# Kernel tuning notes

Hardware: AMD Instinct MI355X
Metric: run time of the kernel (lower is better)

The kernel has to match this reference:

```python
import jax, jax.numpy as jnp
import numpy as np

B, N, D, H = 4, 2048, 1024, 16
HD = D // H
SCALE = D ** -0.5  # NOTE: original scales by dimension**-0.5 (not head_dim**-0.5)


def setup_inputs() -> dict:
    key = jax.random.key(0)
    k1, k2, k3 = jax.random.split(key, 3)
    x = jax.random.normal(k1, (B, N, D), dtype=jnp.float32)
    w_qkv = jax.random.normal(k2, (D, 3 * D), dtype=jnp.float32) * (D ** -0.5)
    w_proj = jax.random.normal(k3, (D, D), dtype=jnp.float32) * (D ** -0.5)
    b_proj = jnp.zeros((D,), dtype=jnp.float32)
    return {"x": x, "w_qkv": w_qkv, "w_proj": w_proj, "b_proj": b_proj}


def reference(x, w_qkv, w_proj, b_proj):
    # qkv projection: [B,N,3D] -> split into q,k,v each [B,H,N,HD]
    qkv = x @ w_qkv
    qkv = qkv.reshape(B, N, 3, H, HD).transpose(2, 0, 3, 1, 4)  # [3,B,H,N,HD]
    q, k, v = qkv[0], qkv[1], qkv[2]
    scores = jnp.einsum('bhid,bhjd->bhij', q, k) * SCALE
    attn = jax.nn.softmax(scores, axis=-1)
    out = jnp.einsum('bhij,bhjd->bhid', attn, v)  # [B,H,N,HD]
    out = out.transpose(0, 2, 1, 3).reshape(B, N, D)
    return out @ w_proj + b_proj
```

## Files before the change

kernel.cpp:

```cpp
#include <hip/hip_runtime.h>
#include <stdint.h>

#define Bdim 4
#define Nseq 2048
#define Dmod 1024
#define Hn   16
#define HD   64
#define SCALE 0.03125f
#define L2E   1.44269504089f

typedef __attribute__((ext_vector_type(8))) short short8;
typedef __attribute__((ext_vector_type(8))) unsigned short ushort8;
typedef __attribute__((ext_vector_type(4))) float f32x4;
typedef __attribute__((ext_vector_type(16))) float f32x16;

typedef __attribute__((address_space(3))) uint32_t lds_u32;
typedef __attribute__((address_space(1))) const uint32_t glob_u32;

static __device__ __forceinline__ void gload_lds16(const unsigned short* g, unsigned short* l) {
    __builtin_amdgcn_global_load_lds((glob_u32*)(const void*)g, (lds_u32*)(void*)l, 16, 0, 0);
}

static __device__ __forceinline__ unsigned short f2bf(float f) {
    union { float f; uint32_t u; } v; v.f = f;
    uint32_t r = (v.u + 0x7FFFu + ((v.u >> 16) & 1u)) >> 16;
    return (unsigned short)r;
}

__global__ __launch_bounds__(256) void cast_x_kernel(const float* __restrict__ in,
                                                     unsigned short* __restrict__ out, int n4) {
    int i = blockIdx.x * blockDim.x + threadIdx.x;
    int stride = gridDim.x * blockDim.x;
    for (; i < n4; i += stride) {
        float4 v = reinterpret_cast<const float4*>(in)[i];
        ushort4 o;
        o.x = f2bf(v.x); o.y = f2bf(v.y); o.z = f2bf(v.z); o.w = f2bf(v.w);
        reinterpret_cast<ushort4*>(out)[i] = o;
    }
}

__global__ void transpose_cast_kernel(const float* __restrict__ in,
                                      unsigned short* __restrict__ out, int R, int C) {
    __shared__ unsigned short t[32][33];
    int c0 = blockIdx.x * 32, r0 = blockIdx.y * 32;
    int tx = threadIdx.x, ty = threadIdx.y;
#pragma unroll
    for (int i = 0; i < 4; ++i)
        t[ty + i*8][tx] = f2bf(in[(size_t)(r0 + ty + i*8) * C + c0 + tx]);
    __syncthreads();
#pragma unroll
    for (int i = 0; i < 4; ++i)
        out[(size_t)(c0 + ty + i*8) * R + r0 + tx] = t[tx][ty + i*8];
}

template<bool OUT_BF16, bool BIAS>
__global__ __launch_bounds__(256) void gemm_bt_kernel(const unsigned short* __restrict__ A,
                                                      const unsigned short* __restrict__ Bt,
                                                      void* __restrict__ Cv,
                                                      const float* __restrict__ bias,
                                                      int M, int N, int K) {
    __shared__ unsigned short Al[128 * 64];
    __shared__ unsigned short Bl[128 * 64];
    int tid = threadIdx.x;
    int lane = tid & 63, wv = tid >> 6;
    int wr = (wv >> 1) * 64, wc = (wv & 1) * 64;
    int lr = lane & 15, lg = lane >> 4, lk = lg * 8;

    int gx = gridDim.x;
    int lin = blockIdx.y * gx + blockIdx.x;
    int cpx = (gx * gridDim.y) >> 3;
    int nl = (lin & 7) * cpx + (lin >> 3);
    int m0 = (nl / gx) * 128, n0 = (nl % gx) * 128;

    int srow = wv * 8 + (lane >> 3);
    int scol = (lane & 7) * 8;
    const unsigned short* ag = A  + (size_t)(m0 + srow) * K + scol;
    const unsigned short* bg = Bt + (size_t)(n0 + srow) * K + scol;
    unsigned short* la = Al + wv * 512;
    unsigned short* lb = Bl + wv * 512;

    f32x4 acc[4][4];
#pragma unroll
    for (int i = 0; i < 4; ++i)
#pragma unroll
        for (int j = 0; j < 4; ++j) acc[i][j] = (f32x4)0.f;

    for (int k0 = 0; k0 < K; k0 += 64) {
        __syncthreads();
#pragma unroll
        for (int i = 0; i < 4; ++i) {
            gload_lds16(ag + (size_t)i * 32 * K + k0, la + i * 2048);
            gload_lds16(bg + (size_t)i * 32 * K + k0, lb + i * 2048);
        }
        __syncthreads();
#pragma unroll
        for (int ks = 0; ks < 2; ++ks) {
            short8 a[4], b[4];
#pragma unroll
            for (int mi = 0; mi < 4; ++mi)
                a[mi] = *reinterpret_cast<const short8*>(Al + (wr + mi*16 + lr) * 64 + ks*32 + lk);
#pragma unroll
            for (int nj = 0; nj < 4; ++nj)
                b[nj] = *reinterpret_cast<const short8*>(Bl + (wc + nj*16 + lr) * 64 + ks*32 + lk);
#pragma unroll
            for (int mi = 0; mi < 4; ++mi)
#pragma unroll
                for (int nj = 0; nj < 4; ++nj)
                    acc[mi][nj] = __builtin_amdgcn_mfma_f32_16x16x32_bf16(a[mi], b[nj], acc[mi][nj], 0, 0, 0);
        }
    }
#pragma unroll
    for (int mi = 0; mi < 4; ++mi) {
#pragma unroll
        for (int nj = 0; nj < 4; ++nj) {
            int r = m0 + wr + mi*16 + lg*4;
            int c = n0 + wc + nj*16 + lr;
            float bv = BIAS ? bias[c] : 0.f;
#pragma unroll
            for (int i = 0; i < 4; ++i) {
                float v = acc[mi][nj][i] + bv;
                if (OUT_BF16)
                    reinterpret_cast<unsigned short*>(Cv)[(size_t)(r + i) * N + c] = f2bf(v);
                else
                    reinterpret_cast<float*>(Cv)[(size_t)(r + i) * N + c] = v;
            }
        }
    }
}

__global__ __launch_bounds__(256) void transpose_v_kernel(const unsigned short* __restrict__ qkv,
                                                          unsigned short* __restrict__ vT) {
    __shared__ unsigned short t[64][68];
    int bh = blockIdx.y, b = bh >> 4, h = bh & 15;
    int j0 = blockIdx.x * 64;
    int tid = threadIdx.x;
#pragma unroll
    for (int p = 0; p < 4; ++p) {
        int e = p * 256 + tid;
        int jj = e >> 4;
        int d4 = (e & 15) * 4;
        const unsigned short* src = qkv + (size_t)(b*Nseq + j0 + jj) * 3072 + 2048 + h*64 + d4;
        ushort4 v = *reinterpret_cast<const ushort4*>(src);
        *reinterpret_cast<ushort4*>(&t[jj][d4]) = v;
    }
    __syncthreads();
#pragma unroll
    for (int p = 0; p < 4; ++p) {
        int e = p * 256 + tid;
        int d = e >> 4;
        int j4 = (e & 15) * 4;
        ushort4 v;
        v.x = t[j4 + 0][d]; v.y = t[j4 + 1][d]; v.z = t[j4 + 2][d]; v.w = t[j4 + 3][d];
        *reinterpret_cast<ushort4*>(vT + ((size_t)bh * 64 + d) * Nseq + j0 + j4) = v;
    }
}

__global__ __launch_bounds__(256, 2) void attn_kernel(const unsigned short* __restrict__ qkv,
                                                      const unsigned short* __restrict__ vT,
                                                      unsigned short* __restrict__ attn_o) {
    __shared__ unsigned short Kl[2 * 64 * 64];
    __shared__ unsigned short Vl[2 * 64 * 64];
    __shared__ unsigned short Pl[4 * 64 * 64];

    int w = blockIdx.x;
    int lid = (w & 7) * 64 + (w >> 3);
    int bh = lid >> 3, qb = lid & 7;
    int b = bh >> 4, h = bh & 15;

    int tid = threadIdx.x, lane = tid & 63, wv = tid >> 6;
    int lr = lane & 31, hi = lane >> 5;
    int q0 = qb * 256 + wv * 64;

    short8 qfA[4], qfB[4];
    {
        const unsigned short* qrowA = qkv + (size_t)(b * Nseq + q0 + lr) * 3072 + h * 64 + hi * 8;
        const unsigned short* qrowB = qrowA + (size_t)32 * 3072;
#pragma unroll
        for (int ks = 0; ks < 4; ++ks) {
            qfA[ks] = *reinterpret_cast<const short8*>(qrowA + ks * 16);
            qfB[ks] = *reinterpret_cast<const short8*>(qrowB + ks * 16);
        }
    }

    float mrunA = -1e30f, lrunA = 0.f, mrunB = -1e30f, lrunB = 0.f;
    f32x16 oA0 = (f32x16)0.f, oA1 = (f32x16)0.f, oB0 = (f32x16)0.f, oB1 = (f32x16)0.f;

    int sr = tid >> 2;
    int sc = (tid & 3) * 32;
    const unsigned short* kg = qkv + (size_t)(b * Nseq + sr) * 3072 + 1024 + h * 64 + sc / 2;
    const unsigned short* vg = vT + ((size_t)(bh * 64 + sr)) * Nseq + sc / 2;
    int swz0 = sr * 128 + ((sc) ^ ((sr & 7) << 4));
    int swz1 = sr * 128 + ((sc + 16) ^ ((sr & 7) << 4));
    int rswz = (lr & 7) << 4;
    char* PlW = (char*)Pl + wv * 8192 + lr * 128;

    {
        ushort8 a0 = *reinterpret_cast<const ushort8*>(kg);
        ushort8 a1 = *reinterpret_cast<const ushort8*>(kg + 8);
        ushort8 a2 = *reinterpret_cast<const ushort8*>(vg);
        ushort8 a3 = *reinterpret_cast<const ushort8*>(vg + 8);
        *reinterpret_cast<ushort8*>((char*)Kl + swz0) = a0;
        *reinterpret_cast<ushort8*>((char*)Kl + swz1) = a1;
        *reinterpret_cast<ushort8*>((char*)Vl + swz0) = a2;
        *reinterpret_cast<ushort8*>((char*)Vl + swz1) = a3;
    }
    ushort8 k0r = *reinterpret_cast<const ushort8*>(kg + (size_t)64 * 3072);
    ushort8 k1r = *reinterpret_cast<const ushort8*>(kg + (size_t)64 * 3072 + 8);
    ushort8 v0r = *reinterpret_cast<const ushort8*>(vg + 64);
    ushort8 v1r = *reinterpret_cast<const ushort8*>(vg + 72);

    int cur = 0;
    for (int jt = 0; jt < Nseq; jt += 64, cur ^= 1) {
        __syncthreads();
        int rb = cur * 8192, wb = rb ^ 8192;

        f32x16 sA0 = (f32x16)0.f, sA1 = (f32x16)0.f, sB0 = (f32x16)0.f, sB1 = (f32x16)0.f;
        __builtin_amdgcn_s_setprio(1);
#pragma unroll
        for (int ks = 0; ks < 4; ++ks) {
            int cb = ks * 32 + hi * 16;
            short8 kf0 = *reinterpret_cast<const short8*>((char*)Kl + rb + lr * 128 + (cb ^ rswz));
            short8 kf1 = *reinterpret_cast<const short8*>((char*)Kl + rb + (lr + 32) * 128 + (cb ^ rswz));
            sA0 = __builtin_amdgcn_mfma_f32_32x32x16_bf16(kf0, qfA[ks], sA0, 0, 0, 0);
            sA1 = __builtin_amdgcn_mfma_f32_32x32x16_bf16(kf1, qfA[ks], sA1, 0, 0, 0);
            sB0 = __builtin_amdgcn_mfma_f32_32x32x16_bf16(kf0, qfB[ks], sB0, 0, 0, 0);
            sB1 = __builtin_amdgcn_mfma_f32_32x32x16_bf16(kf1, qfB[ks], sB1, 0, 0, 0);
        }
        __builtin_amdgcn_s_setprio(0);

        if (jt + 64 < Nseq) {
            *reinterpret_cast<ushort8*>((char*)Kl + wb + swz0) = k0r;
            *reinterpret_cast<ushort8*>((char*)Kl + wb + swz1) = k1r;
            *reinterpret_cast<ushort8*>((char*)Vl + wb + swz0) = v0r;
            *reinterpret_cast<ushort8*>((char*)Vl + wb + swz1) = v1r;
            int jn = jt + 128;
            if (jn < Nseq) {
                k0r = *reinterpret_cast<const ushort8*>(kg + (size_t)jn * 3072);
                k1r = *reinterpret_cast<const ushort8*>(kg + (size_t)jn * 3072 + 8);
                v0r = *reinterpret_cast<const ushort8*>(vg + jn);
                v1r = *reinterpret_cast<const ushort8*>(vg + jn + 8);
            }
        }

        float tA[16], tB[16];
#pragma unroll
        for (int i = 0; i < 16; ++i) { tA[i] = fmaxf(sA0[i], sA1[i]); tB[i] = fmaxf(sB0[i], sB1[i]); }
#pragma unroll
        for (int st = 8; st > 0; st >>= 1)
#pragma unroll
            for (int i = 0; i < st; ++i) { tA[i] = fmaxf(tA[i], tA[i + st]); tB[i] = fmaxf(tB[i], tB[i + st]); }
        float mlocA = fmaxf(tA[0], __shfl_xor(tA[0], 32)) * SCALE;
        float mlocB = fmaxf(tB[0], __shfl_xor(tB[0], 32)) * SCALE;

        if (!__all((mlocA <= mrunA + 8.f) && (mlocB <= mrunB + 8.f))) {
            float mnA = fmaxf(mrunA, mlocA);
            float fA = __builtin_amdgcn_exp2f((mrunA - mnA) * L2E);
            float mnB = fmaxf(mrunB, mlocB);
            float fB = __builtin_amdgcn_exp2f((mrunB - mnB) * L2E);
            lrunA *= fA; lrunB *= fB; mrunA = mnA; mrunB = mnB;
#pragma unroll
            for (int i = 0; i < 16; ++i) {
                oA0[i] *= fA; oA1[i] *= fA; oB0[i] *= fB; oB1[i] *= fB;
            }
        }

        const float c1 = SCALE * L2E;
        float c0A = -mrunA * L2E, c0B = -mrunB * L2E;
        float pA0[16], pA1[16], pB0[16], pB1[16];
#pragma unroll
        for (int i = 0; i < 16; ++i) {
            pA0[i] = __builtin_amdgcn_exp2f(fmaf(sA0[i], c1, c0A));
            pA1[i] = __builtin_amdgcn_exp2f(fmaf(sA1[i], c1, c0A));
            pB0[i] = __builtin_amdgcn_exp2f(fmaf(sB0[i], c1, c0B));
            pB1[i] = __builtin_amdgcn_exp2f(fmaf(sB1[i], c1, c0B));
        }

        uint32_t WA[16], WB[16];
#pragma unroll
        for (int m = 0; m < 8; ++m) {
            asm("v_cvt_pk_bf16_f32 %0, %1, %2" : "=v"(WA[m])   : "v"(pA0[2*m]), "v"(pA0[2*m+1]));
            asm("v_cvt_pk_bf16_f32 %0, %1, %2" : "=v"(WA[8+m]) : "v"(pA1[2*m]), "v"(pA1[2*m+1]));
            asm("v_cvt_pk_bf16_f32 %0, %1, %2" : "=v"(WB[m])   : "v"(pB0[2*m]), "v"(pB0[2*m+1]));
            asm("v_cvt_pk_bf16_f32 %0, %1, %2" : "=v"(WB[8+m]) : "v"(pB1[2*m]), "v"(pB1[2*m+1]));
        }
#pragma unroll
        for (int tt = 0; tt < 8; ++tt) {
            uint64_t valA = (uint64_t)WA[2*tt] | ((uint64_t)WA[2*tt+1] << 32);
            uint64_t valB = (uint64_t)WB[2*tt] | ((uint64_t)WB[2*tt+1] << 32);
            int off = (16*tt + 8*hi) ^ rswz;
            *reinterpret_cast<uint64_t*>(PlW + off) = valA;
            *reinterpret_cast<uint64_t*>(PlW + 4096 + off) = valB;
        }

        float aA[16], aB[16];
#pragma unroll
        for (int i = 0; i < 16; ++i) { aA[i] = pA0[i] + pA1[i]; aB[i] = pB0[i] + pB1[i]; }
#pragma unroll
        for (int st = 8; st > 0; st >>= 1)
#pragma unroll
            for (int i = 0; i < st; ++i) { aA[i] += aA[i + st]; aB[i] += aB[i + st]; }
        lrunA += aA[0] + __shfl_xor(aA[0], 32);
        lrunB += aB[0] + __shfl_xor(aB[0], 32);

        __builtin_amdgcn_s_setprio(1);
#pragma unroll
        for (int ks4 = 0; ks4 < 4; ++ks4) {
            int cb = ks4 * 32 + hi * 16;
            short8 vf0 = *reinterpret_cast<const short8*>((char*)Vl + rb + lr * 128 + (cb ^ rswz));
            short8 vf1 = *reinterpret_cast<const short8*>((char*)Vl + rb + (lr + 32) * 128 + (cb ^ rswz));
            short8 pfA = *reinterpret_cast<const short8*>(PlW + (cb ^ rswz));
            short8 pfB = *reinterpret_cast<const short8*>(PlW + 4096 + (cb ^ rswz));
            oA0 = __builtin_amdgcn_mfma_f32_32x32x16_bf16(vf0, pfA, oA0, 0, 0, 0);
            oA1 = __builtin_amdgcn_mfma_f32_32x32x16_bf16(vf1, pfA, oA1, 0, 0, 0);
            oB0 = __builtin_amdgcn_mfma_f32_32x32x16_bf16(vf0, pfB, oB0, 0, 0, 0);
            oB1 = __builtin_amdgcn_mfma_f32_32x32x16_bf16(vf1, pfB, oB1, 0, 0, 0);
        }
        __builtin_amdgcn_s_setprio(0);
    }

    float invA = 1.f / lrunA, invB = 1.f / lrunB;
    unsigned short* orowA = attn_o + (size_t)(b * Nseq + q0 + lr) * Dmod + h * 64;
    unsigned short* orowB = attn_o + (size_t)(b * Nseq + q0 + 32 + lr) * Dmod + h * 64;
#pragma unroll
    for (int db = 0; db < 2; ++db)
#pragma unroll
        for (int g = 0; g < 4; ++g) {
            int d = db * 32 + 8 * g + 4 * hi;
            ushort4 o4;
            o4.x = f2bf((db ? oA1[4*g+0] : oA0[4*g+0]) * invA);
            o4.y = f2bf((db ? oA1[4*g+1] : oA0[4*g+1]) * invA);
            o4.z = f2bf((db ? oA1[4*g+2] : oA0[4*g+2]) * invA);
            o4.w = f2bf((db ? oA1[4*g+3] : oA0[4*g+3]) * invA);
            *reinterpret_cast<ushort4*>(orowA + d) = o4;
            o4.x = f2bf((db ? oB1[4*g+0] : oB0[4*g+0]) * invB);
            o4.y = f2bf((db ? oB1[4*g+1] : oB0[4*g+1]) * invB);
            o4.z = f2bf((db ? oB1[4*g+2] : oB0[4*g+2]) * invB);
            o4.w = f2bf((db ? oB1[4*g+3] : oB0[4*g+3]) * invB);
            *reinterpret_cast<ushort4*>(orowB + d) = o4;
        }
}

extern "C" void kernel_launch(void* const* d_in, const int* in_sizes, int n_in,
                              void* d_out, int out_size, void* d_ws, size_t ws_size,
                              hipStream_t stream) {
    const float* x      = (const float*)d_in[0];
    const float* w_qkv  = (const float*)d_in[1];
    const float* w_proj = (const float*)d_in[2];
    const float* b_proj = (const float*)d_in[3];
    float* out = (float*)d_out;
    char* ws = (char*)d_ws;

    unsigned short* qkv    = (unsigned short*)(ws);
    unsigned short* vT     = (unsigned short*)(ws + 50331648);
    unsigned short* xb     = (unsigned short*)(ws + 67108864);
    unsigned short* attn_o = xb;
    unsigned short* wqkvT  = (unsigned short*)(ws + 83886080);
    unsigned short* wprojT = (unsigned short*)(ws + 90177536);

    cast_x_kernel<<<2048, 256, 0, stream>>>(x, xb, (Bdim*Nseq*Dmod)/4);
    transpose_cast_kernel<<<dim3(3072/32, 1024/32), dim3(32, 8), 0, stream>>>(w_qkv, wqkvT, 1024, 3072);
    transpose_cast_kernel<<<dim3(1024/32, 1024/32), dim3(32, 8), 0, stream>>>(w_proj, wprojT, 1024, 1024);
    gemm_bt_kernel<true, false><<<dim3(3072/128, 8192/128), 256, 0, stream>>>(
        xb, wqkvT, qkv, nullptr, Bdim*Nseq, 3*Dmod, Dmod);
    transpose_v_kernel<<<dim3(Nseq/64, Bdim*Hn), 256, 0, stream>>>(qkv, vT);
    attn_kernel<<<512, 256, 0, stream>>>(qkv, vT, attn_o);
    gemm_bt_kernel<false, true><<<dim3(1024/128, 8192/128), 256, 0, stream>>>(
        attn_o, wprojT, out, b_proj, Bdim*Nseq, Dmod, Dmod);
}
```

Measured before the change: 226.2 us.

## Fuse V transpose into QKV GEMM epilogue and remap attention LDS layout

The QKV GEMM epilogue now writes the V columns straight into the transposed vT buffer, so the separate transpose_v kernel launch and its extra read/write of V are gone. The attention kernel's K, V and P shared-memory tiles change from an XOR-swizzled row layout to a fragment-major layout where each lane reads a contiguous 16 bytes. This is meant to simplify address math and avoid bank conflicts. The vT stores from the GEMM are 8-byte scattered writes with a large stride, which may cost some write efficiency.

```diff
diff --git a/kernel.cpp b/kernel.cpp
--- a/kernel.cpp
+++ b/kernel.cpp
@@ -53,11 +53,12 @@
         out[(size_t)(c0 + ty + i*8) * R + r0 + tx] = t[tx][ty + i*8];
 }
 
-template<bool OUT_BF16, bool BIAS>
+template<bool OUT_BF16, bool BIAS, bool VSPLIT>
 __global__ __launch_bounds__(256) void gemm_bt_kernel(const unsigned short* __restrict__ A,
                                                       const unsigned short* __restrict__ Bt,
                                                       void* __restrict__ Cv,
                                                       const float* __restrict__ bias,
+                                                      unsigned short* __restrict__ vTp,
                                                       int M, int N, int K) {
     __shared__ unsigned short Al[128 * 64];
     __shared__ unsigned short Bl[128 * 64];
@@ -115,43 +116,28 @@
         for (int nj = 0; nj < 4; ++nj) {
             int r = m0 + wr + mi*16 + lg*4;
             int c = n0 + wc + nj*16 + lr;
-            float bv = BIAS ? bias[c] : 0.f;
-#pragma unroll
-            for (int i = 0; i < 4; ++i) {
-                float v = acc[mi][nj][i] + bv;
-                if (OUT_BF16)
-                    reinterpret_cast<unsigned short*>(Cv)[(size_t)(r + i) * N + c] = f2bf(v);
-                else
-                    reinterpret_cast<float*>(Cv)[(size_t)(r + i) * N + c] = v;
+            if (VSPLIT && c >= 2048) {
+                int cc = c - 2048;
+                int bh = ((r >> 11) << 4) + (cc >> 6);
+                int d = cc & 63;
+                ushort4 o4;
+                o4.x = f2bf(acc[mi][nj][0]);
+                o4.y = f2bf(acc[mi][nj][1]);
+                o4.z = f2bf(acc[mi][nj][2]);
+                o4.w = f2bf(acc[mi][nj][3]);
+                *reinterpret_cast<ushort4*>(vTp + ((size_t)(bh * 64 + d) * 2048) + (r & 2047)) = o4;
+            } else {
+                float bv = BIAS ? bias[c] : 0.f;
+#pragma unroll
+                for (int i = 0; i < 4; ++i) {
+                    float v = acc[mi][nj][i] + bv;
+                    if (OUT_BF16)
+                        reinterpret_cast<unsigned short*>(Cv)[(size_t)(r + i) * N + c] = f2bf(v);
+                    else
+                        reinterpret_cast<float*>(Cv)[(size_t)(r + i) * N + c] = v;
+                }
             }
         }
-    }
-}
-
-__global__ __launch_bounds__(256) void transpose_v_kernel(const unsigned short* __restrict__ qkv,
-                                                          unsigned short* __restrict__ vT) {
-    __shared__ unsigned short t[64][68];
-    int bh = blockIdx.y, b = bh >> 4, h = bh & 15;
-    int j0 = blockIdx.x * 64;
-    int tid = threadIdx.x;
-#pragma unroll
-    for (int p = 0; p < 4; ++p) {
-        int e = p * 256 + tid;
-        int jj = e >> 4;
-        int d4 = (e & 15) * 4;
-        const unsigned short* src = qkv + (size_t)(b*Nseq + j0 + jj) * 3072 + 2048 + h*64 + d4;
-        ushort4 v = *reinterpret_cast<const ushort4*>(src);
-        *reinterpret_cast<ushort4*>(&t[jj][d4]) = v;
-    }
-    __syncthreads();
-#pragma unroll
-    for (int p = 0; p < 4; ++p) {
-        int e = p * 256 + tid;
-        int d = e >> 4;
-        int j4 = (e & 15) * 4;
-        ushort4 v;
-        v.x = t[j4 + 0][d]; v.y = t[j4 + 1][d]; v.z = t[j4 + 2][d]; v.w = t[j4 + 3][d];
-        *reinterpret_cast<ushort4*>(vT + ((size_t)bh * 64 + d) * Nseq + j0 + j4) = v;
     }
 }
 
@@ -186,23 +172,21 @@
     f32x16 oA0 = (f32x16)0.f, oA1 = (f32x16)0.f, oB0 = (f32x16)0.f, oB1 = (f32x16)0.f;
 
     int sr = tid >> 2;
-    int sc = (tid & 3) * 32;
-    const unsigned short* kg = qkv + (size_t)(b * Nseq + sr) * 3072 + 1024 + h * 64 + sc / 2;
-    const unsigned short* vg = vT + ((size_t)(bh * 64 + sr)) * Nseq + sc / 2;
-    int swz0 = sr * 128 + ((sc) ^ ((sr & 7) << 4));
-    int swz1 = sr * 128 + ((sc + 16) ^ ((sr & 7) << 4));
-    int rswz = (lr & 7) << 4;
-    char* PlW = (char*)Pl + wv * 8192 + lr * 128;
+    const unsigned short* kg = qkv + (size_t)(b * Nseq + sr) * 3072 + 1024 + h * 64 + (tid & 3) * 16;
+    const unsigned short* vg = vT + ((size_t)(bh * 64 + sr)) * Nseq + (tid & 3) * 16;
+    int sb = (sr >> 5) * 4096 + (tid & 3) * 1024 + (sr & 31) * 16;
+    char* Pw = (char*)Pl + wv * 8192 + lr * 16 + 8 * hi;
+    char* Pr = (char*)Pl + wv * 8192 + lane * 16;
 
     {
         ushort8 a0 = *reinterpret_cast<const ushort8*>(kg);
         ushort8 a1 = *reinterpret_cast<const ushort8*>(kg + 8);
         ushort8 a2 = *reinterpret_cast<const ushort8*>(vg);
         ushort8 a3 = *reinterpret_cast<const ushort8*>(vg + 8);
-        *reinterpret_cast<ushort8*>((char*)Kl + swz0) = a0;
-        *reinterpret_cast<ushort8*>((char*)Kl + swz1) = a1;
-        *reinterpret_cast<ushort8*>((char*)Vl + swz0) = a2;
-        *reinterpret_cast<ushort8*>((char*)Vl + swz1) = a3;
+        *reinterpret_cast<ushort8*>((char*)Kl + sb) = a0;
+        *reinterpret_cast<ushort8*>((char*)Kl + sb + 512) = a1;
+        *reinterpret_cast<ushort8*>((char*)Vl + sb) = a2;
+        *reinterpret_cast<ushort8*>((char*)Vl + sb + 512) = a3;
     }
     ushort8 k0r = *reinterpret_cast<const ushort8*>(kg + (size_t)64 * 3072);
     ushort8 k1r = *reinterpret_cast<const ushort8*>(kg + (size_t)64 * 3072 + 8);
@@ -218,9 +202,8 @@
         __builtin_amdgcn_s_setprio(1);
 #pragma unroll
         for (int ks = 0; ks < 4; ++ks) {
-            int cb = ks * 32 + hi * 16;
-            short8 kf0 = *reinterpret_cast<const short8*>((char*)Kl + rb + lr * 128 + (cb ^ rswz));
-            short8 kf1 = *reinterpret_cast<const short8*>((char*)Kl + rb + (lr + 32) * 128 + (cb ^ rswz));
+            short8 kf0 = *reinterpret_cast<const short8*>((char*)Kl + rb + ks*1024 + lane*16);
+            short8 kf1 = *reinterpret_cast<const short8*>((char*)Kl + rb + 4096 + ks*1024 + lane*16);
             sA0 = __builtin_amdgcn_mfma_f32_32x32x16_bf16(kf0, qfA[ks], sA0, 0, 0, 0);
             sA1 = __builtin_amdgcn_mfma_f32_32x32x16_bf16(kf1, qfA[ks], sA1, 0, 0, 0);
             sB0 = __builtin_amdgcn_mfma_f32_32x32x16_bf16(kf0, qfB[ks], sB0, 0, 0, 0);
@@ -229,10 +212,10 @@
         __builtin_amdgcn_s_setprio(0);
 
         if (jt + 64 < Nseq) {
-            *reinterpret_cast<ushort8*>((char*)Kl + wb + swz0) = k0r;
-            *reinterpret_cast<ushort8*>((char*)Kl + wb + swz1) = k1r;
-            *reinterpret_cast<ushort8*>((char*)Vl + wb + swz0) = v0r;
-            *reinterpret_cast<ushort8*>((char*)Vl + wb + swz1) = v1r;
+            *reinterpret_cast<ushort8*>((char*)Kl + wb + sb) = k0r;
+            *reinterpret_cast<ushort8*>((char*)Kl + wb + sb + 512) = k1r;
+            *reinterpret_cast<ushort8*>((char*)Vl + wb + sb) = v0r;
+            *reinterpret_cast<ushort8*>((char*)Vl + wb + sb + 512) = v1r;
             int jn = jt + 128;
             if (jn < Nseq) {
                 k0r = *reinterpret_cast<const ushort8*>(kg + (size_t)jn * 3072);
@@ -287,9 +270,9 @@
         for (int tt = 0; tt < 8; ++tt) {
             uint64_t valA = (uint64_t)WA[2*tt] | ((uint64_t)WA[2*tt+1] << 32);
             uint64_t valB = (uint64_t)WB[2*tt] | ((uint64_t)WB[2*tt+1] << 32);
-            int off = (16*tt + 8*hi) ^ rswz;
-            *reinterpret_cast<uint64_t*>(PlW + off) = valA;
-            *reinterpret_cast<uint64_t*>(PlW + 4096 + off) = valB;
+            char* pa = Pw + (tt >> 1) * 1024 + (tt & 1) * 512;
+            *reinterpret_cast<uint64_t*>(pa) = valA;
+            *reinterpret_cast<uint64_t*>(pa + 4096) = valB;
         }
 
         float aA[16], aB[16];
@@ -305,11 +288,10 @@
         __builtin_amdgcn_s_setprio(1);
 #pragma unroll
         for (int ks4 = 0; ks4 < 4; ++ks4) {
-            int cb = ks4 * 32 + hi * 16;
-            short8 vf0 = *reinterpret_cast<const short8*>((char*)Vl + rb + lr * 128 + (cb ^ rswz));
-            short8 vf1 = *reinterpret_cast<const short8*>((char*)Vl + rb + (lr + 32) * 128 + (cb ^ rswz));
-            short8 pfA = *reinterpret_cast<const short8*>(PlW + (cb ^ rswz));
-            short8 pfB = *reinterpret_cast<const short8*>(PlW + 4096 + (cb ^ rswz));
+            short8 vf0 = *reinterpret_cast<const short8*>((char*)Vl + rb + ks4*1024 + lane*16);
+            short8 vf1 = *reinterpret_cast<const short8*>((char*)Vl + rb + 4096 + ks4*1024 + lane*16);
+            short8 pfA = *reinterpret_cast<const short8*>(Pr + ks4*1024);
+            short8 pfB = *reinterpret_cast<const short8*>(Pr + 4096 + ks4*1024);
             oA0 = __builtin_amdgcn_mfma_f32_32x32x16_bf16(vf0, pfA, oA0, 0, 0, 0);
             oA1 = __builtin_amdgcn_mfma_f32_32x32x16_bf16(vf1, pfA, oA1, 0, 0, 0);
             oB0 = __builtin_amdgcn_mfma_f32_32x32x16_bf16(vf0, pfB, oB0, 0, 0, 0);
@@ -360,10 +342,9 @@
     cast_x_kernel<<<2048, 256, 0, stream>>>(x, xb, (Bdim*Nseq*Dmod)/4);
     transpose_cast_kernel<<<dim3(3072/32, 1024/32), dim3(32, 8), 0, stream>>>(w_qkv, wqkvT, 1024, 3072);
     transpose_cast_kernel<<<dim3(1024/32, 1024/32), dim3(32, 8), 0, stream>>>(w_proj, wprojT, 1024, 1024);
-    gemm_bt_kernel<true, false><<<dim3(3072/128, 8192/128), 256, 0, stream>>>(
-        xb, wqkvT, qkv, nullptr, Bdim*Nseq, 3*Dmod, Dmod);
-    transpose_v_kernel<<<dim3(Nseq/64, Bdim*Hn), 256, 0, stream>>>(qkv, vT);
+    gemm_bt_kernel<true, false, true><<<dim3(3072/128, 8192/128), 256, 0, stream>>>(
+        xb, wqkvT, qkv, nullptr, vT, Bdim*Nseq, 3*Dmod, Dmod);
     attn_kernel<<<512, 256, 0, stream>>>(qkv, vT, attn_o);
-    gemm_bt_kernel<false, true><<<dim3(1024/128, 8192/128), 256, 0, stream>>>(
-        attn_o, wprojT, out, b_proj, Bdim*Nseq, Dmod, Dmod);
-}
+    gemm_bt_kernel<false, true, false><<<dim3(1024/128, 8192/128), 256, 0, stream>>>(
+        attn_o, wprojT, out, b_proj, nullptr, Bdim*Nseq, Dmod, Dmod);
+}
```

Measured after the change: 223.9 us. No clear change (-1.0%).
